# Performance work log

Measured on AMD Instinct MI355X. Metric: run time of the kernel, lower is better.

## Reference

```python
import jax, jax.numpy as jnp
import numpy as np

SIGMA = 1.0  # kernel bandwidth (init kwarg)

VS = 4096   # src vertices
VT = 4096   # tar vertices
FS = 8192   # src triangles
FT = 8192   # tar triangles
FR = 8192   # reference triangles


def setup_inputs() -> dict:
    key = jax.random.key(0)
    k0, k1, k2, k3, k4, k5 = jax.random.split(key, 6)
    src_vertices = jax.random.normal(k0, (VS, 3), dtype=jnp.float32)
    src_indices = jax.random.randint(k1, (FS, 3), 0, VS, dtype=jnp.int64)
    tar_vertices = jax.random.normal(k2, (VT, 3), dtype=jnp.float32)
    tar_indices = jax.random.randint(k3, (FT, 3), 0, VT, dtype=jnp.int64)
    ref_normals = 0.1 * jax.random.normal(k4, (FR, 3), dtype=jnp.float32)
    ref_centers = jax.random.normal(k5, (FR, 3), dtype=jnp.float32)
    return {
        "src_vertices": src_vertices,
        "src_indices": src_indices,
        "tar_vertices": tar_vertices,
        "tar_indices": tar_indices,
        "ref_normals": ref_normals,
        "ref_centers": ref_centers,
    }


def _tri_normals_centers(vertices, indices):
    tris = vertices[indices]               # [F, 3, 3]
    a, b, c = tris[:, 0, :], tris[:, 1, :], tris[:, 2, :]
    normals = 0.5 * jnp.cross(a - b, c - b)  # [F, 3]
    centers = tris.sum(axis=1) / 3.0         # [F, 3]
    return normals, centers


def _sqdist(src, tar):
    # d[i, j] = ||tar_i - src_j||^2  -> shape [Nt, Ns]
    s2 = jnp.sum(src * src, axis=-1)  # [Ns]
    t2 = jnp.sum(tar * tar, axis=-1)  # [Nt]
    return t2[:, None] + s2[None, :] - 2.0 * (tar @ src.T)


def _cauchy(d):
    return 1.0 / (1.0 + d / SIGMA) ** 2


def _energy(sn, sc, tn, tc):
    e1 = jnp.sum((sn @ sn.T) * _cauchy(_sqdist(sc, sc)))
    e2 = jnp.sum((tn @ sn.T) * _cauchy(_sqdist(sc, tc)))
    e3 = jnp.sum((tn @ tn.T) * _cauchy(_sqdist(tc, tc)))
    return e1 - 2.0 * e2 + e3


def reference(src_vertices, src_indices, tar_vertices, tar_indices, ref_normals, ref_centers):
    src_n, src_c = _tri_normals_centers(src_vertices, src_indices)
    tar_n, tar_c = _tri_normals_centers(tar_vertices, tar_indices)
    energy = _energy(src_n, src_c, ref_normals, ref_centers)
    energy = energy + _energy(tar_n, tar_c, ref_normals, ref_centers)
    energy = energy + 0.8 * _energy(src_n, src_c, tar_n, tar_c)
    return energy
```

## Files before the change

kernel.cpp:

```cpp
#include <hip/hip_runtime.h>

#define NSEG 8192
#define NPTS (3 * NSEG)
#define NSUP 96
#define NXB  192
#define NYG  13

typedef short bf16x8 __attribute__((ext_vector_type(8)));
typedef float f32x16 __attribute__((ext_vector_type(16)));
typedef unsigned short u16;

__device__ __forceinline__ u16 f2bf(float x) {
    unsigned u = __builtin_bit_cast(unsigned, x);
    return (u16)((u + 0x7FFFu + ((u >> 16) & 1u)) >> 16);
}
__device__ __forceinline__ float bf2f(u16 h) {
    unsigned u = ((unsigned)h) << 16;
    return __builtin_bit_cast(float, u);
}

__device__ __forceinline__ void compute_point(
    int seg, int f,
    const float* __restrict__ sv, const int* __restrict__ si,
    const float* __restrict__ tv, const int* __restrict__ ti,
    const float* __restrict__ rn, const float* __restrict__ rc,
    float& cx, float& cy, float& cz, float& nx, float& ny, float& nz)
{
    if (seg == 2) {
        nx = rn[3*f];   ny = rn[3*f+1]; nz = rn[3*f+2];
        cx = rc[3*f];   cy = rc[3*f+1]; cz = rc[3*f+2];
    } else {
        const float* v  = (seg == 0) ? sv : tv;
        const int*   nd = (seg == 0) ? si : ti;
        int i0 = nd[3*f], i1 = nd[3*f+1], i2 = nd[3*f+2];
        float ax = v[3*i0], ay = v[3*i0+1], az = v[3*i0+2];
        float bx = v[3*i1], by = v[3*i1+1], bz = v[3*i1+2];
        float gx = v[3*i2], gy = v[3*i2+1], gz = v[3*i2+2];
        float ux = ax-bx, uy = ay-by, uz = az-bz;
        float wx = gx-bx, wy = gy-by, wz = gz-bz;
        nx = 0.5f*(uy*wz - uz*wy);
        ny = 0.5f*(uz*wx - ux*wz);
        nz = 0.5f*(ux*wy - uy*wx);
        cx = (ax+bx+gx)*(1.0f/3.0f);
        cy = (ay+by+gy)*(1.0f/3.0f);
        cz = (az+bz+gz)*(1.0f/3.0f);
    }
}

__global__ void setup_feats(const float* __restrict__ sv, const int* __restrict__ si,
                            const float* __restrict__ tv, const int* __restrict__ ti,
                            const float* __restrict__ rn, const float* __restrict__ rc,
                            u16* __restrict__ ws, float* __restrict__ out) {
    int p = blockIdx.x * 256 + threadIdx.x;
    if (p == 0) out[0] = 0.0f;
    if (p >= NPTS) return;
    int seg = p >> 13, f = p & (NSEG - 1);
    float cx, cy, cz, nx, ny, nz;
    compute_point(seg, f, sv, si, tv, ti, rn, rc, cx, cy, cz, nx, ny, nz);

    const u16 ONE = 0x3F80;
    float s = cx*cx + cy*cy + cz*cz;
    u16 chx = f2bf(cx), chy = f2bf(cy), chz = f2bf(cz);
    u16 clx = f2bf(cx - bf2f(chx)), cly = f2bf(cy - bf2f(chy)), clz = f2bf(cz - bf2f(chz));
    u16 sh  = f2bf(s);
    u16 sl  = f2bf(s - bf2f(sh));
    u16 m2hx = f2bf(-2.0f*bf2f(chx)), m2hy = f2bf(-2.0f*bf2f(chy)), m2hz = f2bf(-2.0f*bf2f(chz));
    u16 m2lx = f2bf(-2.0f*bf2f(clx)), m2ly = f2bf(-2.0f*bf2f(cly)), m2lz = f2bf(-2.0f*bf2f(clz));
    u16 nhx = f2bf(nx), nhy = f2bf(ny), nhz = f2bf(nz);
    u16 nlx = f2bf(nx - bf2f(nhx)), nly = f2bf(ny - bf2f(nhy)), nlz = f2bf(nz - bf2f(nhz));

    u16 at[16] = {chx,chy,chz, clx,cly,clz, chx,chy,chz, sh, sl, ONE, ONE, ONE, 0, 0};
    u16 bt[16] = {m2hx,m2hy,m2hz, m2hx,m2hy,m2hz, m2lx,m2ly,m2lz, ONE, ONE, sh, sl, ONE, 0, 0};
    u16 an[16] = {nhx,nhy,nhz, nlx,nly,nlz, nhx,nhy,nhz, 0,0,0,0,0,0,0};
    u16 bn[16] = {nhx,nhy,nhz, nhx,nhy,nhz, nlx,nly,nlz, 0,0,0,0,0,0,0};

    bf16x8* A8 = (bf16x8*)ws;
    bf16x8* B8 = A8 + (size_t)NPTS*4;
    bf16x8 v0, v1, v2, v3;
    #pragma unroll
    for (int k = 0; k < 8; ++k) { v0[k] = (short)at[k]; v1[k] = (short)at[k+8];
                                  v2[k] = (short)an[k]; v3[k] = (short)an[k+8]; }
    A8[(size_t)p*4+0] = v0; A8[(size_t)p*4+1] = v1; A8[(size_t)p*4+2] = v2; A8[(size_t)p*4+3] = v3;
    #pragma unroll
    for (int k = 0; k < 8; ++k) { v0[k] = (short)bt[k]; v1[k] = (short)bt[k+8];
                                  v2[k] = (short)bn[k]; v3[k] = (short)bn[k+8]; }
    B8[(size_t)p*4+0] = v0; B8[(size_t)p*4+1] = v1; B8[(size_t)p*4+2] = v2; B8[(size_t)p*4+3] = v3;
}

__launch_bounds__(256, 3)
__global__ void energy_mfma(const u16* __restrict__ ws, float* __restrict__ out) {
    const int tid  = threadIdx.x;
    const int lane = tid & 63, wid = tid >> 6;
    const int half = lane >> 5, r32 = lane & 31;

    const int bx = blockIdx.x;
    const int X  = bx >> 1;
    const int g  = blockIdx.y;
    const int y0  = (g < 12) ? 4*g : 48;
    const int ycnt = (g < 12) ? 4 : 1;
    const int gi = X >> 5;

    const float Wt[9] = {1.8f, -0.8f, -1.0f,
                        -0.8f,  1.8f, -1.0f,
                        -1.0f, -1.0f,  2.0f};

    const bf16x8* A8 = (const bf16x8*)ws;
    const bf16x8* B8 = A8 + (size_t)NPTS*4;

    const int pi = X*256 + (bx & 1)*128 + wid*32 + r32;
    const bf16x8 at = A8[pi*4 + half];
    const bf16x8 an = A8[pi*4 + 2 + half];

    f32x16 Z;
    #pragma unroll
    for (int k = 0; k < 16; ++k) Z[k] = 0.0f;

    const int lofs = r32*4 + half;

    float acc = 0.0f;
    for (int yy = 0; yy < ycnt; ++yy) {
        const int y = y0 + yy;
        int J = X + y; if (J >= NSUP) J -= NSUP;
        const float mult = (y == 0 || y == 48) ? 1.0f : 2.0f;
        const float w = Wt[gi*3 + (J >> 5)] * mult;

        const int base = J*1024 + lofs;

        bf16x8 btf = B8[base];
        bf16x8 bnf = B8[base + 2];

        float ts0 = 0.0f, ts1 = 0.0f;
        #pragma unroll 2
        for (int jt = 0; jt < 8; ++jt) {
            int nofs = base + ((jt < 7) ? (jt + 1) : jt) * 128;
            bf16x8 nbt = B8[nofs];
            bf16x8 nbn = B8[nofs + 2];

            f32x16 ct = __builtin_amdgcn_mfma_f32_32x32x16_bf16(at, btf, Z, 0, 0, 0);
            f32x16 cn = __builtin_amdgcn_mfma_f32_32x32x16_bf16(an, bnf, Z, 0, 0, 0);

            #pragma unroll
            for (int gq = 0; gq < 4; ++gq) {
                float t0 = ct[4*gq+0], t1 = ct[4*gq+1], t2 = ct[4*gq+2], t3 = ct[4*gq+3];
                float q0 = t0*t0, q1 = t1*t1, q2 = t2*t2, q3 = t3*t3;
                float s01 = q0*q1, s23 = q2*q3;
                float r   = __builtin_amdgcn_rcpf(s01*s23);
                float u   = __builtin_fmaf(cn[4*gq+1], q0, cn[4*gq+0]*q1);
                float v   = __builtin_fmaf(cn[4*gq+3], q2, cn[4*gq+2]*q3);
                float num = __builtin_fmaf(v, s01, u*s23);
                if (gq & 1) ts1 = __builtin_fmaf(num, r, ts1);
                else        ts0 = __builtin_fmaf(num, r, ts0);
            }

            btf = nbt; bnf = nbn;
        }
        acc = __builtin_fmaf(w, ts0 + ts1, acc);
    }

    for (int off = 32; off; off >>= 1) acc += __shfl_down(acc, off, 64);
    __shared__ float partial[4];
    if ((tid & 63) == 0) partial[wid] = acc;
    __syncthreads();
    if (tid == 0)
        atomicAdd(out, (partial[0] + partial[1]) + (partial[2] + partial[3]));
}

extern "C" void kernel_launch(void* const* d_in, const int* in_sizes, int n_in,
                              void* d_out, int out_size, void* d_ws, size_t ws_size,
                              hipStream_t stream) {
    const float* sv = (const float*)d_in[0];
    const int*   si = (const int*)d_in[1];
    const float* tv = (const float*)d_in[2];
    const int*   ti = (const int*)d_in[3];
    const float* rn = (const float*)d_in[4];
    const float* rc = (const float*)d_in[5];
    float* out = (float*)d_out;
    u16*   ws  = (u16*)d_ws;

    setup_feats<<<NPTS/256, 256, 0, stream>>>(sv, si, tv, ti, rn, rc, ws, out);
    dim3 grid(NXB, NYG);
    energy_mfma<<<grid, 256, 0, stream>>>(ws, out);
}
```

Baseline: 118.6 us.

## Software-pipeline MFMA with epilogue across flattened tiles; split setup into A/B threads

New measurement: 118.9 us. About the same (+0.3%).

```diff
diff --git a/kernel.cpp b/kernel.cpp
--- a/kernel.cpp
+++ b/kernel.cpp
@@ -51,9 +51,10 @@
                             const float* __restrict__ tv, const int* __restrict__ ti,
                             const float* __restrict__ rn, const float* __restrict__ rc,
                             u16* __restrict__ ws, float* __restrict__ out) {
-    int p = blockIdx.x * 256 + threadIdx.x;
-    if (p == 0) out[0] = 0.0f;
-    if (p >= NPTS) return;
+    int gid = blockIdx.x * 256 + threadIdx.x;
+    if (gid == 0) out[0] = 0.0f;
+    const int rec = (gid >= NPTS);
+    const int p   = rec ? gid - NPTS : gid;
     int seg = p >> 13, f = p & (NSEG - 1);
     float cx, cy, cz, nx, ny, nz;
     compute_point(seg, f, sv, si, tv, ti, rn, rc, cx, cy, cz, nx, ny, nz);
@@ -64,27 +65,32 @@
     u16 clx = f2bf(cx - bf2f(chx)), cly = f2bf(cy - bf2f(chy)), clz = f2bf(cz - bf2f(chz));
     u16 sh  = f2bf(s);
     u16 sl  = f2bf(s - bf2f(sh));
-    u16 m2hx = f2bf(-2.0f*bf2f(chx)), m2hy = f2bf(-2.0f*bf2f(chy)), m2hz = f2bf(-2.0f*bf2f(chz));
-    u16 m2lx = f2bf(-2.0f*bf2f(clx)), m2ly = f2bf(-2.0f*bf2f(cly)), m2lz = f2bf(-2.0f*bf2f(clz));
     u16 nhx = f2bf(nx), nhy = f2bf(ny), nhz = f2bf(nz);
     u16 nlx = f2bf(nx - bf2f(nhx)), nly = f2bf(ny - bf2f(nhy)), nlz = f2bf(nz - bf2f(nhz));
 
-    u16 at[16] = {chx,chy,chz, clx,cly,clz, chx,chy,chz, sh, sl, ONE, ONE, ONE, 0, 0};
-    u16 bt[16] = {m2hx,m2hy,m2hz, m2hx,m2hy,m2hz, m2lx,m2ly,m2lz, ONE, ONE, sh, sl, ONE, 0, 0};
-    u16 an[16] = {nhx,nhy,nhz, nlx,nly,nlz, nhx,nhy,nhz, 0,0,0,0,0,0,0};
-    u16 bn[16] = {nhx,nhy,nhz, nhx,nhy,nhz, nlx,nly,nlz, 0,0,0,0,0,0,0};
-
     bf16x8* A8 = (bf16x8*)ws;
     bf16x8* B8 = A8 + (size_t)NPTS*4;
+    u16 r0[16], r1[16];
+    if (!rec) {
+        u16 at[16] = {chx,chy,chz, clx,cly,clz, chx,chy,chz, sh, sl, ONE, ONE, ONE, 0, 0};
+        u16 an[16] = {nhx,nhy,nhz, nlx,nly,nlz, nhx,nhy,nhz, 0,0,0,0,0,0,0};
+        #pragma unroll
+        for (int k = 0; k < 16; ++k) { r0[k] = at[k]; r1[k] = an[k]; }
+    } else {
+        u16 m2hx = f2bf(-2.0f*bf2f(chx)), m2hy = f2bf(-2.0f*bf2f(chy)), m2hz = f2bf(-2.0f*bf2f(chz));
+        u16 m2lx = f2bf(-2.0f*bf2f(clx)), m2ly = f2bf(-2.0f*bf2f(cly)), m2lz = f2bf(-2.0f*bf2f(clz));
+        u16 bt[16] = {m2hx,m2hy,m2hz, m2hx,m2hy,m2hz, m2lx,m2ly,m2lz, ONE, ONE, sh, sl, ONE, 0, 0};
+        u16 bn[16] = {nhx,nhy,nhz, nhx,nhy,nhz, nlx,nly,nlz, 0,0,0,0,0,0,0};
+        #pragma unroll
+        for (int k = 0; k < 16; ++k) { r0[k] = bt[k]; r1[k] = bn[k]; }
+    }
+    bf16x8* dst = rec ? B8 : A8;
     bf16x8 v0, v1, v2, v3;
     #pragma unroll
-    for (int k = 0; k < 8; ++k) { v0[k] = (short)at[k]; v1[k] = (short)at[k+8];
-                                  v2[k] = (short)an[k]; v3[k] = (short)an[k+8]; }
-    A8[(size_t)p*4+0] = v0; A8[(size_t)p*4+1] = v1; A8[(size_t)p*4+2] = v2; A8[(size_t)p*4+3] = v3;
-    #pragma unroll
-    for (int k = 0; k < 8; ++k) { v0[k] = (short)bt[k]; v1[k] = (short)bt[k+8];
-                                  v2[k] = (short)bn[k]; v3[k] = (short)bn[k+8]; }
-    B8[(size_t)p*4+0] = v0; B8[(size_t)p*4+1] = v1; B8[(size_t)p*4+2] = v2; B8[(size_t)p*4+3] = v3;
+    for (int k = 0; k < 8; ++k) { v0[k] = (short)r0[k]; v1[k] = (short)r0[k+8];
+                                  v2[k] = (short)r1[k]; v3[k] = (short)r1[k+8]; }
+    dst[(size_t)p*4+0] = v0; dst[(size_t)p*4+1] = v1;
+    dst[(size_t)p*4+2] = v2; dst[(size_t)p*4+3] = v3;
 }
 
 __launch_bounds__(256, 3)
@@ -96,13 +102,13 @@
     const int bx = blockIdx.x;
     const int X  = bx >> 1;
     const int g  = blockIdx.y;
-    const int y0  = (g < 12) ? 4*g : 48;
-    const int ycnt = (g < 12) ? 4 : 1;
+    const int y0   = (g < 12) ? 4*g : 48;
+    const int total = ((g < 12) ? 4 : 1) * 8;
     const int gi = X >> 5;
 
-    const float Wt[9] = {1.8f, -0.8f, -1.0f,
-                        -0.8f,  1.8f, -1.0f,
-                        -1.0f, -1.0f,  2.0f};
+    const float w0 = (gi == 0) ? 1.8f : (gi == 1 ? -0.8f : -1.0f);
+    const float w1 = (gi == 0) ? -0.8f : (gi == 1 ? 1.8f : -1.0f);
+    const float w2 = (gi == 2) ? 2.0f : -1.0f;
 
     const bf16x8* A8 = (const bf16x8*)ws;
     const bf16x8* B8 = A8 + (size_t)NPTS*4;
@@ -117,45 +123,69 @@
 
     const int lofs = r32*4 + half;
 
+    #define TILE_OFS(idx, Jv)  ({ int _y = y0 + ((idx) >> 3);                      \
+                                  int _J = X + _y; if (_J >= NSUP) _J -= NSUP;     \
+                                  Jv = _J; _J*1024 + ((idx) & 7)*128 + lofs; })
+    #define TILE_W(idx, Jv)    ({ int _y = y0 + ((idx) >> 3);                      \
+                                  float _m = (_y == 0 || _y == 48) ? 1.0f : 2.0f;  \
+                                  int _gj = (Jv) >> 5;                             \
+                                  ((_gj == 0) ? w0 : (_gj == 1 ? w1 : w2)) * _m; })
+
+    int J0; int o0 = TILE_OFS(0, J0);
+    bf16x8 btf = B8[o0], bnf = B8[o0 + 2];
+    f32x16 ct_p = __builtin_amdgcn_mfma_f32_32x32x16_bf16(at, btf, Z, 0, 0, 0);
+    f32x16 cn_p = __builtin_amdgcn_mfma_f32_32x32x16_bf16(an, bnf, Z, 0, 0, 0);
+    float w_p = TILE_W(0, J0);
+    int J1; int o1 = TILE_OFS(1, J1);
+    btf = B8[o1]; bnf = B8[o1 + 2];
+
     float acc = 0.0f;
-    for (int yy = 0; yy < ycnt; ++yy) {
-        const int y = y0 + yy;
-        int J = X + y; if (J >= NSUP) J -= NSUP;
-        const float mult = (y == 0 || y == 48) ? 1.0f : 2.0f;
-        const float w = Wt[gi*3 + (J >> 5)] * mult;
-
-        const int base = J*1024 + lofs;
-
-        bf16x8 btf = B8[base];
-        bf16x8 bnf = B8[base + 2];
+    #pragma unroll 2
+    for (int idx = 1; idx < total; ++idx) {
+        f32x16 ct_n = __builtin_amdgcn_mfma_f32_32x32x16_bf16(at, btf, Z, 0, 0, 0);
+        f32x16 cn_n = __builtin_amdgcn_mfma_f32_32x32x16_bf16(an, bnf, Z, 0, 0, 0);
+        int Jc; float w_n = TILE_W(idx, (TILE_OFS(idx, Jc), Jc));
+
+        int nid = (idx + 1 < total) ? idx + 1 : idx;
+        int Jn; int on = TILE_OFS(nid, Jn);
+        btf = B8[on]; bnf = B8[on + 2];
 
         float ts0 = 0.0f, ts1 = 0.0f;
-        #pragma unroll 2
-        for (int jt = 0; jt < 8; ++jt) {
-            int nofs = base + ((jt < 7) ? (jt + 1) : jt) * 128;
-            bf16x8 nbt = B8[nofs];
-            bf16x8 nbn = B8[nofs + 2];
-
-            f32x16 ct = __builtin_amdgcn_mfma_f32_32x32x16_bf16(at, btf, Z, 0, 0, 0);
-            f32x16 cn = __builtin_amdgcn_mfma_f32_32x32x16_bf16(an, bnf, Z, 0, 0, 0);
-
-            #pragma unroll
-            for (int gq = 0; gq < 4; ++gq) {
-                float t0 = ct[4*gq+0], t1 = ct[4*gq+1], t2 = ct[4*gq+2], t3 = ct[4*gq+3];
-                float q0 = t0*t0, q1 = t1*t1, q2 = t2*t2, q3 = t3*t3;
-                float s01 = q0*q1, s23 = q2*q3;
-                float r   = __builtin_amdgcn_rcpf(s01*s23);
-                float u   = __builtin_fmaf(cn[4*gq+1], q0, cn[4*gq+0]*q1);
-                float v   = __builtin_fmaf(cn[4*gq+3], q2, cn[4*gq+2]*q3);
-                float num = __builtin_fmaf(v, s01, u*s23);
-                if (gq & 1) ts1 = __builtin_fmaf(num, r, ts1);
-                else        ts0 = __builtin_fmaf(num, r, ts0);
-            }
-
-            btf = nbt; bnf = nbn;
+        #pragma unroll
+        for (int gq = 0; gq < 4; ++gq) {
+            float t0 = ct_p[4*gq+0], t1 = ct_p[4*gq+1], t2 = ct_p[4*gq+2], t3 = ct_p[4*gq+3];
+            float q0 = t0*t0, q1 = t1*t1, q2 = t2*t2, q3 = t3*t3;
+            float s01 = q0*q1, s23 = q2*q3;
+            float r   = __builtin_amdgcn_rcpf(s01*s23);
+            float u   = __builtin_fmaf(cn_p[4*gq+1], q0, cn_p[4*gq+0]*q1);
+            float v   = __builtin_fmaf(cn_p[4*gq+3], q2, cn_p[4*gq+2]*q3);
+            float num = __builtin_fmaf(v, s01, u*s23);
+            if (gq & 1) ts1 = __builtin_fmaf(num, r, ts1);
+            else        ts0 = __builtin_fmaf(num, r, ts0);
         }
-        acc = __builtin_fmaf(w, ts0 + ts1, acc);
-    }
+        acc = __builtin_fmaf(w_p, ts0 + ts1, acc);
+
+        ct_p = ct_n; cn_p = cn_n; w_p = w_n;
+    }
+
+    {
+        float ts0 = 0.0f, ts1 = 0.0f;
+        #pragma unroll
+        for (int gq = 0; gq < 4; ++gq) {
+            float t0 = ct_p[4*gq+0], t1 = ct_p[4*gq+1], t2 = ct_p[4*gq+2], t3 = ct_p[4*gq+3];
+            float q0 = t0*t0, q1 = t1*t1, q2 = t2*t2, q3 = t3*t3;
+            float s01 = q0*q1, s23 = q2*q3;
+            float r   = __builtin_amdgcn_rcpf(s01*s23);
+            float u   = __builtin_fmaf(cn_p[4*gq+1], q0, cn_p[4*gq+0]*q1);
+            float v   = __builtin_fmaf(cn_p[4*gq+3], q2, cn_p[4*gq+2]*q3);
+            float num = __builtin_fmaf(v, s01, u*s23);
+            if (gq & 1) ts1 = __builtin_fmaf(num, r, ts1);
+            else        ts0 = __builtin_fmaf(num, r, ts0);
+        }
+        acc = __builtin_fmaf(w_p, ts0 + ts1, acc);
+    }
+    #undef TILE_OFS
+    #undef TILE_W
 
     for (int off = 32; off; off >>= 1) acc += __shfl_down(acc, off, 64);
     __shared__ float partial[4];
@@ -177,7 +207,7 @@
     float* out = (float*)d_out;
     u16*   ws  = (u16*)d_ws;
 
-    setup_feats<<<NPTS/256, 256, 0, stream>>>(sv, si, tv, ti, rn, rc, ws, out);
+    setup_feats<<<2*NPTS/256, 256, 0, stream>>>(sv, si, tv, ti, rn, rc, ws, out);
     dim3 grid(NXB, NYG);
     energy_mfma<<<grid, 256, 0, stream>>>(ws, out);
 }
```
